# Performance work log

Hardware: AMD Instinct MI355X
Metric: run time of the kernel (lower is better)

Reference implementation:

```python
import jax, jax.numpy as jnp
import numpy as np

D = 768  # in_channels == out_channels (forced by residual + shared LayerNorm)
B, S = 8, 2048


def setup_inputs() -> dict:
    key = jax.random.key(0)
    ks = jax.random.split(key, 5)
    x = jax.random.normal(ks[0], (B, S, D), dtype=jnp.float32)
    # LayerNorm params
    ln_g = jnp.ones((D,), dtype=jnp.float32)
    ln_b = jnp.zeros((D,), dtype=jnp.float32)
    # Q/K linear params (torch Linear: y = x @ W.T + b)
    scale = 1.0 / np.sqrt(D)
    Wq = jax.random.uniform(ks[1], (D, D), jnp.float32, -scale, scale)
    bq = jax.random.uniform(ks[2], (D,), jnp.float32, -scale, scale)
    Wk = jax.random.uniform(ks[3], (D, D), jnp.float32, -scale, scale)
    bk = jax.random.uniform(ks[4], (D,), jnp.float32, -scale, scale)
    return {"x": x, "ln_g": ln_g, "ln_b": ln_b, "Wq": Wq, "bq": bq, "Wk": Wk, "bk": bk}


def _layernorm(x, g, b, eps=1e-5):
    mu = jnp.mean(x, axis=-1, keepdims=True)
    var = jnp.mean(jnp.square(x - mu), axis=-1, keepdims=True)
    return (x - mu) * jax.lax.rsqrt(var + eps) * g + b


def reference(x, ln_g, ln_b, Wq, bq, Wk, bk):
    origin = x
    xn = _layernorm(x, ln_g, ln_b)
    Q = xn @ Wq.T + bq  # [B,S,D]
    K = xn @ Wk.T + bk  # [B,S,D]
    scores = jnp.einsum('bsd,btd->bst', Q, K) / jnp.sqrt(jnp.asarray(D, x.dtype))
    attn = jax.nn.softmax(scores, axis=-1)  # [B,S,S]
    out = jnp.einsum('bst,btd->bsd', attn, origin) + origin
    # note: original then computes relu(layernorm(out)) but returns `out` (dead code)
    return out
```

## Files before the change

kernel.cpp:

```cpp
#include <hip/hip_runtime.h>

typedef __bf16 bf16;
typedef __bf16 v8bf __attribute__((ext_vector_type(8)));
typedef __bf16 v4bf __attribute__((ext_vector_type(4)));
typedef float  v4f  __attribute__((ext_vector_type(4)));

__device__ __forceinline__ void gload_lds16(const void* g, void* l) {
    __builtin_amdgcn_global_load_lds(
        (const __attribute__((address_space(1))) void*)g,
        (__attribute__((address_space(3))) void*)l, 16, 0, 0);
}

#define MFMA16(a, b, c) __builtin_amdgcn_mfma_f32_16x16x32_bf16((a), (b), (c), 0, 0, 0)

__global__ __launch_bounds__(256)
void ln_cast(const float* __restrict__ x, const float* __restrict__ g,
             const float* __restrict__ b, bf16* __restrict__ xn,
             bf16* __restrict__ xv, float* __restrict__ L)
{
    const long row = blockIdx.x;
    const float* xr = x + row * 768;
    const int tid = threadIdx.x;
    const int wave = tid >> 6, lane = tid & 63;

    if (row < 64) L[row * 256 + tid] = 0.0f;

    float a0 = xr[tid], a1 = xr[tid + 256], a2 = xr[tid + 512];
    float s = a0 + a1 + a2;
    #pragma unroll
    for (int off = 32; off; off >>= 1) s += __shfl_xor(s, off);
    __shared__ float sh[4], sh2[4];
    if (!lane) sh[wave] = s;
    __syncthreads();
    const float mu = (sh[0] + sh[1] + sh[2] + sh[3]) * (1.0f / 768.0f);

    float d0 = a0 - mu, d1 = a1 - mu, d2 = a2 - mu;
    float ss = d0 * d0 + d1 * d1 + d2 * d2;
    #pragma unroll
    for (int off = 32; off; off >>= 1) ss += __shfl_xor(ss, off);
    if (!lane) sh2[wave] = ss;
    __syncthreads();
    const float var = (sh2[0] + sh2[1] + sh2[2] + sh2[3]) * (1.0f / 768.0f);
    const float rstd = rsqrtf(var + 1e-5f);

    bf16* xnr = xn + row * 768;
    bf16* xvr = xv + row * 768;
    xnr[tid]       = (bf16)(d0 * rstd * g[tid]       + b[tid]);
    xnr[tid + 256] = (bf16)(d1 * rstd * g[tid + 256] + b[tid + 256]);
    xnr[tid + 512] = (bf16)(d2 * rstd * g[tid + 512] + b[tid + 512]);
    xvr[tid]       = (bf16)a0;
    xvr[tid + 256] = (bf16)a1;
    xvr[tid + 512] = (bf16)a2;
}

__global__ __launch_bounds__(256)
void cvt_w(const float* __restrict__ Wq, const float* __restrict__ Wk,
           bf16* __restrict__ Wcat)
{
    const int z = blockIdx.y;
    const float* src = z ? Wk : Wq;
    bf16* dst = Wcat + (long)z * 768 * 768;
    const int i = (blockIdx.x * 256 + threadIdx.x) * 4;
    const float4 v = *(const float4*)(src + i);
    v4bf o = {(bf16)v.x, (bf16)v.y, (bf16)v.z, (bf16)v.w};
    *(v4bf*)(dst + i) = o;
}

__global__ __launch_bounds__(256)
void transpose_bf(const bf16* __restrict__ in, bf16* __restrict__ outT)
{
    __shared__ __attribute__((aligned(16))) bf16 tile[64 * 64];
    const int t0 = blockIdx.x * 64, d0 = blockIdx.y * 64;
    in   += (long)blockIdx.z * 2048 * 768;
    outT += (long)blockIdx.z * 768 * 2048;
    const int tid = threadIdx.x;

    #pragma unroll
    for (int it = 0; it < 2; ++it) {
        const int lin = it * 256 + tid;
        const int r = lin >> 3;
        const int g = lin & 7;
        const int pg = g ^ (r & 7) ^ ((r >> 3) & 7);
        v8bf v = *(const v8bf*)(in + (long)(t0 + r) * 768 + d0 + g * 8);
        *(v8bf*)(tile + r * 64 + pg * 8) = v;
    }
    __syncthreads();
    #pragma unroll
    for (int it = 0; it < 2; ++it) {
        const int lin = it * 256 + tid;
        const int dd = lin >> 3;
        const int tb = lin & 7;
        v8bf o;
        #pragma unroll
        for (int j = 0; j < 8; ++j) {
            const int t = tb * 8 + j;
            const int pg = (dd >> 3) ^ (t & 7) ^ ((t >> 3) & 7);
            o[j] = tile[t * 64 + pg * 8 + (dd & 7)];
        }
        *(v8bf*)(outT + (long)(d0 + dd) * 2048 + t0 + tb * 8) = o;
    }
}

__global__ __launch_bounds__(256)
void gemm_qk(const bf16* __restrict__ A, const bf16* __restrict__ W,
             const float* __restrict__ bq, const float* __restrict__ bk,
             float qscale, bf16* __restrict__ Qb, bf16* __restrict__ Kb)
{
    __shared__ __attribute__((aligned(16))) bf16 As[2][128 * 32];
    __shared__ __attribute__((aligned(16))) bf16 Bs[2][128 * 32];

    const int bx = blockIdx.x;
    const int r = bx & 7, j = bx >> 3;
    const int m0 = (r * 16 + j / 12) * 128;
    const int n0 = (j % 12) * 128;

    const int tid = threadIdx.x, wave = tid >> 6, lane = tid & 63;
    const bf16* Ab = A + (long)m0 * 768;
    const bf16* Bb = W + (long)n0 * 768;

    const int lrow = lane >> 2;
    const int lk   = (lane & 3) * 8;
    const int wm = (wave >> 1) * 64, wn = (wave & 1) * 64;
    const int lr = lane & 15, lq = lane >> 4;

    v4f acc[4][4] = {};

    for (int kk = 0; kk < 768; kk += 64) {
        #pragma unroll
        for (int p = 0; p < 2; ++p)
            #pragma unroll
            for (int it = 0; it < 2; ++it) {
                const int c = it * 4 + wave;
                const int row = c * 16 + lrow;
                gload_lds16(Ab + (long)row * 768 + kk + p * 32 + lk,
                            (char*)As[p] + c * 1024);
                gload_lds16(Bb + (long)row * 768 + kk + p * 32 + lk,
                            (char*)Bs[p] + c * 1024);
            }
        __syncthreads();

        #pragma unroll
        for (int p = 0; p < 2; ++p) {
            v8bf af[4], bfr[4];
            #pragma unroll
            for (int i = 0; i < 4; ++i)
                af[i] = *(const v8bf*)(As[p] + (wm + i * 16 + lr) * 32 + lq * 8);
            #pragma unroll
            for (int jj = 0; jj < 4; ++jj)
                bfr[jj] = *(const v8bf*)(Bs[p] + (wn + jj * 16 + lr) * 32 + lq * 8);
            #pragma unroll
            for (int i = 0; i < 4; ++i)
                #pragma unroll
                for (int jj = 0; jj < 4; ++jj)
                    acc[i][jj] = MFMA16(af[i], bfr[jj], acc[i][jj]);
        }
        __syncthreads();
    }

    const bool isQ = (n0 < 768);
    const float* bias = isQ ? bq : bk;
    const float sc = isQ ? qscale : 1.0f;
    bf16* C = isQ ? Qb : Kb;
    const int c0 = isQ ? n0 : n0 - 768;

    #pragma unroll
    for (int i = 0; i < 4; ++i) {
        #pragma unroll
        for (int rr = 0; rr < 4; ++rr) {
            const int row = m0 + wm + i * 16 + lq * 4 + rr;
            #pragma unroll
            for (int jj = 0; jj < 4; ++jj) {
                const int col = c0 + wn + jj * 16 + lr;
                C[(long)row * 768 + col] = (bf16)((acc[i][jj][rr] + bias[col]) * sc);
            }
        }
    }
}

__global__ __launch_bounds__(512, 2)
void gemm_scores(const bf16* __restrict__ Q, const bf16* __restrict__ K,
                 bf16* __restrict__ E, float* __restrict__ L)
{
    __shared__ __attribute__((aligned(16))) bf16 lds[4][16384];

    const int bx = blockIdx.x;
    const int batch = bx & 7, j = bx >> 3;
    const int m0 = (j >> 3) * 256, n0 = (j & 7) * 256;

    const bf16* Ag = Q + (long)batch * 2048 * 768 + (long)m0 * 768;
    const bf16* Bg = K + (long)batch * 2048 * 768 + (long)n0 * 768;
    bf16* C = E + (long)batch * 2048 * 2048;
    float* Lb = L + (long)batch * 2048;

    const int tid = threadIdx.x, wv = tid >> 6, lane = tid & 63;
    const int wr = wv >> 2, wc = wv & 3;
    const int lr = lane & 15, lq = lane >> 4;

    auto stageA = [&](int h, int a) {
        const int lin = (wv * 2 + a) * 64 + lane;
        const int r = lin >> 2, pc = lin & 3;
        gload_lds16(Ag + (long)r * 768 + h * 32 + ((pc ^ (r & 3)) << 3),
                    (char*)lds[h & 3] + lin * 16);
    };
    auto stageB = [&](int h, int a) {
        const int lin = (wv * 2 + a) * 64 + lane;
        const int r = lin >> 2, pc = lin & 3;
        gload_lds16(Bg + (long)r * 768 + h * 32 + ((pc ^ (r & 3)) << 3),
                    (char*)lds[h & 3] + 16384 + lin * 16);
    };
    auto rdA = [&](int h, int mf) -> v8bf {
        const int r = wr * 128 + mf * 16 + lr;
        return *(const v8bf*)(lds[h & 3] + r * 32 + ((lq ^ (r & 3)) << 3));
    };
    auto rdB = [&](int h, int nf) -> v8bf {
        const int r = wc * 64 + nf * 16 + lr;
        return *(const v8bf*)(lds[h & 3] + 8192 + r * 32 + ((lq ^ (r & 3)) << 3));
    };

    v8bf a0[4], a1[4], b0[4], b1[4];
    v4f acc[8][4] = {};
    const int NT = 12;

    stageA(0, 0); stageA(0, 1); stageB(0, 0); stageB(0, 1);
    stageA(1, 0); stageA(1, 1); stageB(1, 0); stageB(1, 1);
    asm volatile("s_waitcnt vmcnt(4)" ::: "memory");
    __builtin_amdgcn_s_barrier();
    #pragma unroll
    for (int i = 0; i < 4; ++i) a0[i] = rdA(0, i);
    #pragma unroll
    for (int jn = 0; jn < 4; ++jn) b0[jn] = rdB(0, jn);

    for (int t = 0; t < NT; ++t) {
        const int h0 = 2 * t, h1 = 2 * t + 1, h2 = 2 * t + 2, h3 = 2 * t + 3;
        const bool pre = (t + 1 < NT);

        #pragma unroll
        for (int i = 0; i < 4; ++i) a1[i] = rdA(h0, 4 + i);
        if (pre) { stageA(h2, 0); stageA(h2, 1); }
        __builtin_amdgcn_s_setprio(1);
        #pragma unroll
        for (int i = 0; i < 4; ++i)
            #pragma unroll
            for (int jn = 0; jn < 4; ++jn)
                acc[i][jn] = MFMA16(a0[i], b0[jn], acc[i][jn]);
        __builtin_amdgcn_s_setprio(0);
        asm volatile("s_waitcnt vmcnt(2)" ::: "memory");
        __builtin_amdgcn_s_barrier();

        #pragma unroll
        for (int i = 0; i < 4; ++i) a0[i] = rdA(h1, i);
        #pragma unroll
        for (int jn = 0; jn < 4; ++jn) b1[jn] = rdB(h1, jn);
        if (pre) { stageB(h2, 0); stageB(h2, 1); }
        __builtin_amdgcn_s_setprio(1);
        #pragma unroll
        for (int i = 0; i < 4; ++i)
            #pragma unroll
            for (int jn = 0; jn < 4; ++jn)
                acc[4 + i][jn] = MFMA16(a1[i], b0[jn], acc[4 + i][jn]);
        __builtin_amdgcn_s_setprio(0);
        asm volatile("" ::: "memory");
        __builtin_amdgcn_s_barrier();

        #pragma unroll
        for (int i = 0; i < 4; ++i) a1[i] = rdA(h1, 4 + i);
        if (pre) { stageA(h3, 0); stageA(h3, 1); }
        __builtin_amdgcn_s_setprio(1);
        #pragma unroll
        for (int i = 0; i < 4; ++i)
            #pragma unroll
            for (int jn = 0; jn < 4; ++jn)
                acc[i][jn] = MFMA16(a0[i], b1[jn], acc[i][jn]);
        __builtin_amdgcn_s_setprio(0);
        asm volatile("s_waitcnt vmcnt(2)" ::: "memory");
        __builtin_amdgcn_s_barrier();

        if (pre) {
            #pragma unroll
            for (int i = 0; i < 4; ++i) a0[i] = rdA(h2, i);
            #pragma unroll
            for (int jn = 0; jn < 4; ++jn) b0[jn] = rdB(h2, jn);
            stageB(h3, 0); stageB(h3, 1);
        }
        __builtin_amdgcn_s_setprio(1);
        #pragma unroll
        for (int i = 0; i < 4; ++i)
            #pragma unroll
            for (int jn = 0; jn < 4; ++jn)
                acc[4 + i][jn] = MFMA16(a1[i], b1[jn], acc[4 + i][jn]);
        __builtin_amdgcn_s_setprio(0);
        asm volatile("" ::: "memory");
        __builtin_amdgcn_s_barrier();
    }

    #pragma unroll
    for (int i = 0; i < 8; ++i) {
        #pragma unroll
        for (int rr = 0; rr < 4; ++rr) {
            const int row = m0 + wr * 128 + i * 16 + lq * 4 + rr;
            float e[4], rs = 0.f;
            #pragma unroll
            for (int jn = 0; jn < 4; ++jn) {
                e[jn] = __expf(acc[i][jn][rr]);
                rs += e[jn];
            }
            #pragma unroll
            for (int off = 1; off < 16; off <<= 1) rs += __shfl_xor(rs, off);
            if (lr == 0) atomicAdd(&Lb[row], rs);
            #pragma unroll
            for (int jn = 0; jn < 4; ++jn) {
                const int col = n0 + wc * 64 + jn * 16 + lr;
                C[(long)row * 2048 + col] = (bf16)e[jn];
            }
        }
    }
}

__global__ __launch_bounds__(512, 2)
void gemm_pv(const bf16* __restrict__ P, const bf16* __restrict__ VT,
             const float* __restrict__ L, const float* __restrict__ Xres,
             float* __restrict__ Out)
{
    __shared__ __attribute__((aligned(16))) bf16 lds[4][16384];

    const int bx = blockIdx.x;
    const int batch = bx & 7, j = bx >> 3;
    const int m0 = (j >> 1) * 128;
    const int n0 = (j & 1) * 384;

    const bf16* Ag = P  + (long)batch * 2048 * 2048 + (long)m0 * 2048;
    const bf16* Bg = VT + (long)batch * 768 * 2048  + (long)n0 * 2048;
    const float* Lb = L + (long)batch * 2048;
    const float* Xr = Xres + (long)batch * 2048 * 768;
    float* O = Out + (long)batch * 2048 * 768;

    const int tid = threadIdx.x, wv = tid >> 6, lane = tid & 63;
    const int wr = wv >> 2, wc = wv & 3;
    const int lr = lane & 15, lq = lane >> 4;

    auto stageA = [&](int h) {
        const int lin = wv * 64 + lane;
        const int r = lin >> 2, pc = lin & 3;
        gload_lds16(Ag + (long)r * 2048 + h * 32 + ((pc ^ (r & 3)) << 3),
                    (char*)lds[h & 3] + lin * 16);
    };
    auto stageB = [&](int h, int a) {
        const int lin = (wv * 3 + a) * 64 + lane;
        const int r = lin >> 2, pc = lin & 3;
        gload_lds16(Bg + (long)r * 2048 + h * 32 + ((pc ^ (r & 3)) << 3),
                    (char*)lds[h & 3] + 8192 + lin * 16);
    };
    auto rdA = [&](int h, int mf) -> v8bf {
        const int r = wr * 64 + mf * 16 + lr;
        return *(const v8bf*)(lds[h & 3] + r * 32 + ((lq ^ (r & 3)) << 3));
    };
    auto rdB = [&](int h, int nf) -> v8bf {
        const int r = wc * 96 + nf * 16 + lr;
        return *(const v8bf*)(lds[h & 3] + 4096 + r * 32 + ((lq ^ (r & 3)) << 3));
    };

    v8bf a0[4], a1[4], bL[3], bH[3];
    v4f acc[4][6] = {};
    const int NT = 32;

    stageA(0); stageB(0, 0); stageB(0, 1); stageB(0, 2);
    stageA(1); stageB(1, 0); stageB(1, 1); stageB(1, 2);
    asm volatile("s_waitcnt vmcnt(4)" ::: "memory");
    __builtin_amdgcn_s_barrier();
    #pragma unroll
    for (int i = 0; i < 4; ++i) a0[i] = rdA(0, i);
    #pragma unroll
    for (int jn = 0; jn < 3; ++jn) bL[jn] = rdB(0, jn);

    for (int t = 0; t < NT; ++t) {
        const int h0 = 2 * t, h1 = 2 * t + 1, h2 = 2 * t + 2, h3 = 2 * t + 3;
        const bool pre = (t + 1 < NT);

        #pragma unroll
        for (int jn = 0; jn < 3; ++jn) bH[jn] = rdB(h0, 3 + jn);
        if (pre) { stageA(h2); stageB(h2, 0); }
        __builtin_amdgcn_s_setprio(1);
        #pragma unroll
        for (int i = 0; i < 4; ++i)
            #pragma unroll
            for (int jn = 0; jn < 3; ++jn)
                acc[i][jn] = MFMA16(a0[i], bL[jn], acc[i][jn]);
        __builtin_amdgcn_s_setprio(0);
        asm volatile("s_waitcnt vmcnt(2)" ::: "memory");
        __builtin_amdgcn_s_barrier();

        #pragma unroll
        for (int i = 0; i < 4; ++i) a1[i] = rdA(h1, i);
        #pragma unroll
        for (int jn = 0; jn < 3; ++jn) bL[jn] = rdB(h1, jn);
        if (pre) { stageB(h2, 1); stageB(h2, 2); }
        __builtin_amdgcn_s_setprio(1);
        #pragma unroll
        for (int i = 0; i < 4; ++i)
            #pragma unroll
            for (int jn = 0; jn < 3; ++jn)
                acc[i][3 + jn] = MFMA16(a0[i], bH[jn], acc[i][3 + jn]);
        __builtin_amdgcn_s_setprio(0);
        asm volatile("" ::: "memory");
        __builtin_amdgcn_s_barrier();

        #pragma unroll
        for (int jn = 0; jn < 3; ++jn) bH[jn] = rdB(h1, 3 + jn);
        if (pre) { stageA(h3); stageB(h3, 0); }
        __builtin_amdgcn_s_setprio(1);
        #pragma unroll
        for (int i = 0; i < 4; ++i)
            #pragma unroll
            for (int jn = 0; jn < 3; ++jn)
                acc[i][jn] = MFMA16(a1[i], bL[jn], acc[i][jn]);
        __builtin_amdgcn_s_setprio(0);
        asm volatile("s_waitcnt vmcnt(2)" ::: "memory");
        __builtin_amdgcn_s_barrier();

        if (pre) {
            #pragma unroll
            for (int i = 0; i < 4; ++i) a0[i] = rdA(h2, i);
            #pragma unroll
            for (int jn = 0; jn < 3; ++jn) bL[jn] = rdB(h2, jn);
            stageB(h3, 1); stageB(h3, 2);
        }
        __builtin_amdgcn_s_setprio(1);
        #pragma unroll
        for (int i = 0; i < 4; ++i)
            #pragma unroll
            for (int jn = 0; jn < 3; ++jn)
                acc[i][3 + jn] = MFMA16(a1[i], bH[jn], acc[i][3 + jn]);
        __builtin_amdgcn_s_setprio(0);
        asm volatile("" ::: "memory");
        __builtin_amdgcn_s_barrier();
    }

    #pragma unroll
    for (int i = 0; i < 4; ++i) {
        #pragma unroll
        for (int rr = 0; rr < 4; ++rr) {
            const int row = m0 + wr * 64 + i * 16 + lq * 4 + rr;
            const float invL = 1.0f / Lb[row];
            #pragma unroll
            for (int jn = 0; jn < 6; ++jn) {
                const int col = n0 + wc * 96 + jn * 16 + lr;
                const long idx = (long)row * 768 + col;
                O[idx] = acc[i][jn][rr] * invL + Xr[idx];
            }
        }
    }
}

extern "C" void kernel_launch(void* const* d_in, const int* in_sizes, int n_in,
                              void* d_out, int out_size, void* d_ws, size_t ws_size,
                              hipStream_t stream)
{
    const float* x    = (const float*)d_in[0];
    const float* ln_g = (const float*)d_in[1];
    const float* ln_b = (const float*)d_in[2];
    const float* Wq   = (const float*)d_in[3];
    const float* bq   = (const float*)d_in[4];
    const float* Wk   = (const float*)d_in[5];
    const float* bk   = (const float*)d_in[6];
    float* out = (float*)d_out;

    const long R = 8L * 2048;
    char* ws = (char*)d_ws;
    size_t off = 0;
    auto take = [&](size_t bytes) -> char* {
        char* p = ws + off;
        off += (bytes + 255) & ~(size_t)255;
        return p;
    };
    bf16*  xn   = (bf16*)take(R * 768 * 2);
    bf16*  xv   = (bf16*)take(R * 768 * 2);
    bf16*  Qb   = (bf16*)take(R * 768 * 2);
    bf16*  Kb   = (bf16*)take(R * 768 * 2);
    bf16*  Wcat = (bf16*)take(1536L * 768 * 2);
    float* Lrow = (float*)take(R * 4);
    bf16*  Sc   = (bf16*)take(8L * 2048 * 2048 * 2);

    ln_cast<<<R, 256, 0, stream>>>(x, ln_g, ln_b, xn, xv, Lrow);
    cvt_w<<<dim3(576, 2), 256, 0, stream>>>(Wq, Wk, Wcat);

    const float qscale = 0.036084391824351615f;
    gemm_qk<<<1536, 256, 0, stream>>>(xn, Wcat, bq, bk, qscale, Qb, Kb);

    bf16* xvT = xn;
    transpose_bf<<<dim3(32, 12, 8), 256, 0, stream>>>(xv, xvT);

    gemm_scores<<<512, 512, 0, stream>>>(Qb, Kb, Sc, Lrow);
    gemm_pv<<<256, 512, 0, stream>>>(Sc, xvT, Lrow, x, out);
}
```

Baseline: 316.3 us.

## Rewrite QK projection GEMM with pipelined 128x384 tiles and stronger LDS swizzle

The Q/K projection GEMM moves from a simple double-buffered 128x128 tile kernel with full barriers to the same 4-stage software-pipelined structure the scores and PV kernels use. It now runs 512-thread blocks on 128x384 tiles, interleaves async global-to-LDS loads with MFMA, and raises wave priority around the MFMA groups. The LDS XOR swizzle is extended with a second row-bit term in all three GEMMs to cut bank conflicts on fragment reads. The trade-off is fewer, larger blocks (512 instead of 1536), which may hurt load balance, plus more register use per thread.

Result: faster. 307.5 us (-2.8%).

```diff
diff --git a/kernel.cpp b/kernel.cpp
--- a/kernel.cpp
+++ b/kernel.cpp
@@ -101,61 +101,126 @@
     }
 }
 
-__global__ __launch_bounds__(256)
+__global__ __launch_bounds__(512, 2)
 void gemm_qk(const bf16* __restrict__ A, const bf16* __restrict__ W,
              const float* __restrict__ bq, const float* __restrict__ bk,
              float qscale, bf16* __restrict__ Qb, bf16* __restrict__ Kb)
 {
-    __shared__ __attribute__((aligned(16))) bf16 As[2][128 * 32];
-    __shared__ __attribute__((aligned(16))) bf16 Bs[2][128 * 32];
+    __shared__ __attribute__((aligned(16))) bf16 lds[4][16384];
 
     const int bx = blockIdx.x;
-    const int r = bx & 7, j = bx >> 3;
-    const int m0 = (r * 16 + j / 12) * 128;
-    const int n0 = (j % 12) * 128;
-
-    const int tid = threadIdx.x, wave = tid >> 6, lane = tid & 63;
-    const bf16* Ab = A + (long)m0 * 768;
-    const bf16* Bb = W + (long)n0 * 768;
-
-    const int lrow = lane >> 2;
-    const int lk   = (lane & 3) * 8;
-    const int wm = (wave >> 1) * 64, wn = (wave & 1) * 64;
+    const int wg = (bx & 7) * 64 + (bx >> 3);
+    const int m0 = (wg >> 2) * 128;
+    const int n0 = (wg & 3) * 384;
+
+    const bf16* Ag = A + (long)m0 * 768;
+    const bf16* Bg = W + (long)n0 * 768;
+
+    const int tid = threadIdx.x, wv = tid >> 6, lane = tid & 63;
+    const int wr = wv >> 2, wc = wv & 3;
     const int lr = lane & 15, lq = lane >> 4;
 
-    v4f acc[4][4] = {};
-
-    for (int kk = 0; kk < 768; kk += 64) {
-        #pragma unroll
-        for (int p = 0; p < 2; ++p)
-            #pragma unroll
-            for (int it = 0; it < 2; ++it) {
-                const int c = it * 4 + wave;
-                const int row = c * 16 + lrow;
-                gload_lds16(Ab + (long)row * 768 + kk + p * 32 + lk,
-                            (char*)As[p] + c * 1024);
-                gload_lds16(Bb + (long)row * 768 + kk + p * 32 + lk,
-                            (char*)Bs[p] + c * 1024);
-            }
-        __syncthreads();
-
-        #pragma unroll
-        for (int p = 0; p < 2; ++p) {
-            v8bf af[4], bfr[4];
-            #pragma unroll
-            for (int i = 0; i < 4; ++i)
-                af[i] = *(const v8bf*)(As[p] + (wm + i * 16 + lr) * 32 + lq * 8);
-            #pragma unroll
-            for (int jj = 0; jj < 4; ++jj)
-                bfr[jj] = *(const v8bf*)(Bs[p] + (wn + jj * 16 + lr) * 32 + lq * 8);
-            #pragma unroll
-            for (int i = 0; i < 4; ++i)
-                #pragma unroll
-                for (int jj = 0; jj < 4; ++jj)
-                    acc[i][jj] = MFMA16(af[i], bfr[jj], acc[i][jj]);
-        }
-        __syncthreads();
-    }
+    auto stageA = [&](int h) {
+        const int lin = wv * 64 + lane;
+        const int r = lin >> 2, pc = lin & 3;
+        const int g = pc ^ (r & 3) ^ ((r >> 2) & 3);
+        gload_lds16(Ag + (long)r * 768 + h * 32 + (g << 3),
+                    (char*)lds[h & 3] + lin * 16);
+    };
+    auto stageB = [&](int h, int a) {
+        const int lin = (wv * 3 + a) * 64 + lane;
+        const int r = lin >> 2, pc = lin & 3;
+        const int g = pc ^ (r & 3) ^ ((r >> 2) & 3);
+        gload_lds16(Bg + (long)r * 768 + h * 32 + (g << 3),
+                    (char*)lds[h & 3] + 8192 + lin * 16);
+    };
+    auto rdA = [&](int h, int mf) -> v8bf {
+        const int r = wr * 64 + mf * 16 + lr;
+        return *(const v8bf*)(lds[h & 3] + r * 32 +
+                              ((lq ^ (r & 3) ^ ((r >> 2) & 3)) << 3));
+    };
+    auto rdB = [&](int h, int nf) -> v8bf {
+        const int r = wc * 96 + nf * 16 + lr;
+        return *(const v8bf*)(lds[h & 3] + 4096 + r * 32 +
+                              ((lq ^ (r & 3) ^ ((r >> 2) & 3)) << 3));
+    };
+
+    v8bf a0[4], a1[4], bL[3], bH[3];
+    v4f acc[4][6] = {};
+    const int NT = 12;
+
+    stageA(0); stageB(0, 0); stageB(0, 1); stageB(0, 2);
+    stageA(1); stageB(1, 0); stageB(1, 1); stageB(1, 2);
+    asm volatile("s_waitcnt vmcnt(4)" ::: "memory");
+    __builtin_amdgcn_s_barrier();
+    #pragma unroll
+    for (int i = 0; i < 4; ++i) a0[i] = rdA(0, i);
+    #pragma unroll
+    for (int jn = 0; jn < 3; ++jn) bL[jn] = rdB(0, jn);
+
+    for (int t = 0; t < NT; ++t) {
+        const int h0 = 2 * t, h1 = 2 * t + 1, h2 = 2 * t + 2, h3 = 2 * t + 3;
+        const bool pre = (t + 1 < NT);
+
+        #pragma unroll
+        for (int jn = 0; jn < 3; ++jn) bH[jn] = rdB(h0, 3 + jn);
+        if (pre) { stageA(h2); stageB(h2, 0); }
+        __builtin_amdgcn_s_setprio(1);
+        #pragma unroll
+        for (int i = 0; i < 4; ++i)
+            #pragma unroll
+            for (int jn = 0; jn < 3; ++jn)
+                acc[i][jn] = MFMA16(a0[i], bL[jn], acc[i][jn]);
+        __builtin_amdgcn_s_setprio(0);
+        asm volatile("s_waitcnt vmcnt(2)" ::: "memory");
+        __builtin_amdgcn_s_barrier();
+
+        #pragma unroll
+        for (int i = 0; i < 4; ++i) a1[i] = rdA(h1, i);
+        #pragma unroll
+        for (int jn = 0; jn < 3; ++jn) bL[jn] = rdB(h1, jn);
+        if (pre) { stageB(h2, 1); stageB(h2, 2); }
+        __builtin_amdgcn_s_setprio(1);
+        #pragma unroll
+        for (int i = 0; i < 4; ++i)
+            #pragma unroll
+            for (int jn = 0; jn < 3; ++jn)
+                acc[i][3 + jn] = MFMA16(a0[i], bH[jn], acc[i][3 + jn]);
+        __builtin_amdgcn_s_setprio(0);
+        asm volatile("" ::: "memory");
+        __builtin_amdgcn_s_barrier();
+
+        #pragma unroll
+        for (int jn = 0; jn < 3; ++jn) bH[jn] = rdB(h1, 3 + jn);
+        if (pre) { stageA(h3); stageB(h3, 0); }
+        __builtin_amdgcn_s_setprio(1);
+        #pragma unroll
+        for (int i = 0; i < 4; ++i)
+            #pragma unroll
+            for (int jn = 0; jn < 3; ++jn)
+                acc[i][jn] = MFMA16(a1[i], bL[jn], acc[i][jn]);
+        __builtin_amdgcn_s_setprio(0);
+        asm volatile("s_waitcnt vmcnt(2)" ::: "memory");
+        __builtin_amdgcn_s_barrier();
+
+        if (pre) {
+            #pragma unroll
+            for (int i = 0; i < 4; ++i) a0[i] = rdA(h2, i);
+            #pragma unroll
+            for (int jn = 0; jn < 3; ++jn) bL[jn] = rdB(h2, jn);
+            stageB(h3, 1); stageB(h3, 2);
+        }
+        __builtin_amdgcn_s_setprio(1);
+        #pragma unroll
+        for (int i = 0; i < 4; ++i)
+            #pragma unroll
+            for (int jn = 0; jn < 3; ++jn)
+                acc[i][3 + jn] = MFMA16(a1[i], bH[jn], acc[i][3 + jn]);
+        __builtin_amdgcn_s_setprio(0);
+        asm volatile("" ::: "memory");
+        __builtin_amdgcn_s_barrier();
+    }
+    asm volatile("s_waitcnt vmcnt(0)" ::: "memory");
 
     const bool isQ = (n0 < 768);
     const float* bias = isQ ? bq : bk;
@@ -167,11 +232,11 @@
     for (int i = 0; i < 4; ++i) {
         #pragma unroll
         for (int rr = 0; rr < 4; ++rr) {
-            const int row = m0 + wm + i * 16 + lq * 4 + rr;
-            #pragma unroll
-            for (int jj = 0; jj < 4; ++jj) {
-                const int col = c0 + wn + jj * 16 + lr;
-                C[(long)row * 768 + col] = (bf16)((acc[i][jj][rr] + bias[col]) * sc);
+            const int row = m0 + wr * 64 + i * 16 + lq * 4 + rr;
+            #pragma unroll
+            for (int jn = 0; jn < 6; ++jn) {
+                const int col = c0 + wc * 96 + jn * 16 + lr;
+                C[(long)row * 768 + col] = (bf16)((acc[i][jn][rr] + bias[col]) * sc);
             }
         }
     }
@@ -199,22 +264,26 @@
     auto stageA = [&](int h, int a) {
         const int lin = (wv * 2 + a) * 64 + lane;
         const int r = lin >> 2, pc = lin & 3;
-        gload_lds16(Ag + (long)r * 768 + h * 32 + ((pc ^ (r & 3)) << 3),
+        const int g = pc ^ (r & 3) ^ ((r >> 2) & 3);
+        gload_lds16(Ag + (long)r * 768 + h * 32 + (g << 3),
                     (char*)lds[h & 3] + lin * 16);
     };
     auto stageB = [&](int h, int a) {
         const int lin = (wv * 2 + a) * 64 + lane;
         const int r = lin >> 2, pc = lin & 3;
-        gload_lds16(Bg + (long)r * 768 + h * 32 + ((pc ^ (r & 3)) << 3),
+        const int g = pc ^ (r & 3) ^ ((r >> 2) & 3);
+        gload_lds16(Bg + (long)r * 768 + h * 32 + (g << 3),
                     (char*)lds[h & 3] + 16384 + lin * 16);
     };
     auto rdA = [&](int h, int mf) -> v8bf {
         const int r = wr * 128 + mf * 16 + lr;
-        return *(const v8bf*)(lds[h & 3] + r * 32 + ((lq ^ (r & 3)) << 3));
+        return *(const v8bf*)(lds[h & 3] + r * 32 +
+                              ((lq ^ (r & 3) ^ ((r >> 2) & 3)) << 3));
     };
     auto rdB = [&](int h, int nf) -> v8bf {
         const int r = wc * 64 + nf * 16 + lr;
-        return *(const v8bf*)(lds[h & 3] + 8192 + r * 32 + ((lq ^ (r & 3)) << 3));
+        return *(const v8bf*)(lds[h & 3] + 8192 + r * 32 +
+                              ((lq ^ (r & 3) ^ ((r >> 2) & 3)) << 3));
     };
 
     v8bf a0[4], a1[4], b0[4], b1[4];
@@ -341,22 +410,26 @@
     auto stageA = [&](int h) {
         const int lin = wv * 64 + lane;
         const int r = lin >> 2, pc = lin & 3;
-        gload_lds16(Ag + (long)r * 2048 + h * 32 + ((pc ^ (r & 3)) << 3),
+        const int g = pc ^ (r & 3) ^ ((r >> 2) & 3);
+        gload_lds16(Ag + (long)r * 2048 + h * 32 + (g << 3),
                     (char*)lds[h & 3] + lin * 16);
     };
     auto stageB = [&](int h, int a) {
         const int lin = (wv * 3 + a) * 64 + lane;
         const int r = lin >> 2, pc = lin & 3;
-        gload_lds16(Bg + (long)r * 2048 + h * 32 + ((pc ^ (r & 3)) << 3),
+        const int g = pc ^ (r & 3) ^ ((r >> 2) & 3);
+        gload_lds16(Bg + (long)r * 2048 + h * 32 + (g << 3),
                     (char*)lds[h & 3] + 8192 + lin * 16);
     };
     auto rdA = [&](int h, int mf) -> v8bf {
         const int r = wr * 64 + mf * 16 + lr;
-        return *(const v8bf*)(lds[h & 3] + r * 32 + ((lq ^ (r & 3)) << 3));
+        return *(const v8bf*)(lds[h & 3] + r * 32 +
+                              ((lq ^ (r & 3) ^ ((r >> 2) & 3)) << 3));
     };
     auto rdB = [&](int h, int nf) -> v8bf {
         const int r = wc * 96 + nf * 16 + lr;
-        return *(const v8bf*)(lds[h & 3] + 4096 + r * 32 + ((lq ^ (r & 3)) << 3));
+        return *(const v8bf*)(lds[h & 3] + 4096 + r * 32 +
+                              ((lq ^ (r & 3) ^ ((r >> 2) & 3)) << 3));
     };
 
     v8bf a0[4], a1[4], bL[3], bH[3];
@@ -484,7 +557,7 @@
     cvt_w<<<dim3(576, 2), 256, 0, stream>>>(Wq, Wk, Wcat);
 
     const float qscale = 0.036084391824351615f;
-    gemm_qk<<<1536, 256, 0, stream>>>(xn, Wcat, bq, bk, qscale, Qb, Kb);
+    gemm_qk<<<512, 512, 0, stream>>>(xn, Wcat, bq, bk, qscale, Qb, Kb);
 
     bf16* xvT = xn;
     transpose_bf<<<dim3(32, 12, 8), 256, 0, stream>>>(xv, xvT);
```
